# Optimization experiments

Hardware: AMD Instinct MI355X
Metric: run time of the kernel (lower is better)

## Reference

```python
import jax, jax.numpy as jnp
import numpy as np

D_MODEL = 1024
N_HEADS = 16


def setup_inputs() -> dict:
    key = jax.random.key(0)
    ks = jax.random.split(key, 5)
    B, T, C = 4, 2048, D_MODEL
    x = jax.random.normal(ks[0], (B, T, C), dtype=jnp.float32)
    W_attn = jax.random.normal(ks[1], (C, 3 * C), dtype=jnp.float32) * (1.0 / np.sqrt(C))
    b_attn = jnp.zeros((3 * C,), dtype=jnp.float32)
    W_proj = jax.random.normal(ks[2], (C, C), dtype=jnp.float32) * (1.0 / np.sqrt(C))
    b_proj = jnp.zeros((C,), dtype=jnp.float32)
    return {"x": x, "W_attn": W_attn, "b_attn": b_attn, "W_proj": W_proj, "b_proj": b_proj}


def reference(x, W_attn, b_attn, W_proj, b_proj):
    B, T, C = x.shape
    H = N_HEADS
    hd = C // H
    qkv = x @ W_attn + b_attn                      # [B,T,3C]
    q, k, v = jnp.split(qkv, 3, axis=2)
    # [B,T,C] -> [B,H,T,hd]
    q = q.reshape(B, T, H, hd).transpose(0, 2, 1, 3)
    k = k.reshape(B, T, H, hd).transpose(0, 2, 1, 3)
    v = v.reshape(B, T, H, hd).transpose(0, 2, 1, 3)
    scale = 1.0 / jnp.sqrt(jnp.float32(hd))
    attn = jnp.einsum('bhqd,bhkd->bhqk', q, k) * scale
    causal = jnp.tril(jnp.ones((T, T), dtype=bool))
    attn = jnp.where(causal[None, None], attn, -jnp.inf)
    w = jax.nn.softmax(attn, axis=-1)
    ctx = jnp.einsum('bhqk,bhkd->bhqd', w, v)      # [B,H,T,hd]
    ctx = ctx.transpose(0, 2, 1, 3).reshape(B, T, C)
    return ctx @ W_proj + b_proj
```

## Files before the change

### kernel.cpp

```cpp
#include <hip/hip_runtime.h>
#include <hip/hip_bf16.h>

typedef __bf16 bf16x8 __attribute__((ext_vector_type(8)));
typedef __bf16 bf16x4 __attribute__((ext_vector_type(4)));
typedef float f32x4 __attribute__((ext_vector_type(4)));

#define MFMA(A, B, C) __builtin_amdgcn_mfma_f32_16x16x32_bf16((A), (B), (C), 0, 0, 0)

#if __has_builtin(__builtin_amdgcn_exp2f)
#define EXP2(x) __builtin_amdgcn_exp2f(x)
#else
#define EXP2(x) exp2f(x)
#endif

#define T_SEQ 2048
#define BATCH 4
#define CDIM  1024
#define HEADS 16
#define HD    64
#define MROWS (BATCH * T_SEQ)
#define QK_SCALE 0.18033688011112042f
#define KTILES (CDIM / 64)

__device__ __forceinline__ void async_ld16(const __bf16* g, __bf16* l) {
    __builtin_amdgcn_global_load_lds(
        (const __attribute__((address_space(1))) void*)g,
        (__attribute__((address_space(3))) void*)l, 16, 0, 0);
}

__global__ __launch_bounds__(256) void conv_transpose(const float* __restrict__ src,
                                                      __bf16* __restrict__ dst,
                                                      int R, int C)
{
    __shared__ float tile[32][33];
    int c0 = blockIdx.x * 32, r0 = blockIdx.y * 32;
    int tx = threadIdx.x, ty = threadIdx.y;
#pragma unroll
    for (int i = 0; i < 4; i++)
        tile[ty + i * 8][tx] = src[(long)(r0 + ty + i * 8) * C + c0 + tx];
    __syncthreads();
#pragma unroll
    for (int i = 0; i < 4; i++)
        dst[(long)(c0 + ty + i * 8) * R + r0 + tx] = (__bf16)tile[tx][ty + i * 8];
}

__global__ __launch_bounds__(256) void conv_bf16(const float* __restrict__ src,
                                                 __bf16* __restrict__ dst)
{
    long i = ((long)blockIdx.x * 256 + threadIdx.x) * 8;
    f32x4 f0 = ((const f32x4*)(src + i))[0];
    f32x4 f1 = ((const f32x4*)(src + i))[1];
    bf16x8 v;
#pragma unroll
    for (int j = 0; j < 4; j++) { v[j] = (__bf16)f0[j]; v[4 + j] = (__bf16)f1[j]; }
    *(bf16x8*)(dst + i) = v;
}

__global__ __launch_bounds__(256) void vtrans(const __bf16* __restrict__ qkv,
                                              __bf16* __restrict__ vt)
{
    __shared__ __bf16 tile[32][33];
    int bh = blockIdx.z;
    int b = bh >> 4, h = bh & 15;
    int t0 = blockIdx.x * 32, d0 = blockIdx.y * 32;
    int tx = threadIdx.x, ty = threadIdx.y;
#pragma unroll
    for (int i = 0; i < 4; i++)
        tile[ty + i * 8][tx] =
            qkv[(long)(b * T_SEQ + t0 + ty + i * 8) * (3 * CDIM) + 2 * CDIM + h * HD + d0 + tx];
    __syncthreads();
#pragma unroll
    for (int i = 0; i < 4; i++)
        vt[(long)(bh * HD + d0 + ty + i * 8) * T_SEQ + t0 + tx] = tile[tx][ty + i * 8];
}


#define QS_ALO(p, kt)                                                            \
    do {                                                                         \
        async_ld16(Asrc + (long)(kt) * 64, &Ab[p][sdst]);                        \
        async_ld16(Asrc + (long)128 * CDIM + (kt) * 64, &Ab[p][8192 + sdst]);    \
    } while (0)
#define QS_AHI(p, kt)                                                            \
    do {                                                                         \
        async_ld16(Asrc + (long)64 * CDIM + (kt) * 64, &Ab[p][4096 + sdst]);     \
        async_ld16(Asrc + (long)192 * CDIM + (kt) * 64, &Ab[p][12288 + sdst]);   \
    } while (0)
#define QS_B(p, kt)                                                              \
    do {                                                                         \
        async_ld16(Bsrc + (long)(kt) * 64, &Bb[p][sdst]);                        \
        async_ld16(Bsrc + (long)64 * CDIM + (kt) * 64, &Bb[p][4096 + sdst]);     \
        async_ld16(Bsrc + (long)128 * CDIM + (kt) * 64, &Bb[p][8192 + sdst]);    \
    } while (0)

__global__ __launch_bounds__(512, 2) void gemm_qkv(const __bf16* __restrict__ A,
                                                   const __bf16* __restrict__ Bt,
                                                   const float* __restrict__ bias,
                                                   __bf16* __restrict__ C)
{
    __shared__ __attribute__((aligned(16))) __bf16 Ab[2][256 * 64];
    __shared__ __attribute__((aligned(16))) __bf16 Bb[2][192 * 64];

    const int bid = (int)blockIdx.x;
    const int swz = (bid & 7) * 64 + (bid >> 3);
    const int n0 = (swz & 15) * 192;
    const int m0 = (swz >> 4) * 256;

    const int t = threadIdx.x;
    const int wave = t >> 6, lane = t & 63;
    const int quad = lane >> 4, l15 = lane & 15;
    const int wm = wave >> 2, wn = wave & 3;

    const int srow = t >> 3;
    const int scol = ((t & 7) * 8) ^ ((srow & 7) << 3);
    const int sdst = srow * 64 + (t & 7) * 8;
    const __bf16* Asrc = A + (long)(m0 + srow) * CDIM + scol;
    const __bf16* Bsrc = Bt + (long)(n0 + srow) * CDIM + scol;

    const int kx0 = (quad * 8) ^ ((l15 & 7) << 3);
    const int kx1 = (32 + quad * 8) ^ ((l15 & 7) << 3);
    const int aro = (wm * 128 + l15) * 64;
    const int bro = (wn * 48 + l15) * 64;

    f32x4 acc[8][3] = {};
    bf16x8 A0[4][2], A1[4][2], B0[2][2], B1[2];

    QS_ALO(0, 0); QS_AHI(0, 0); QS_B(0, 0);
    QS_ALO(1, 1); QS_AHI(1, 1); QS_B(1, 1);
    asm volatile("s_waitcnt vmcnt(7)" ::: "memory");
    __builtin_amdgcn_s_barrier();
#pragma unroll
    for (int mf = 0; mf < 4; mf++) {
        A0[mf][0] = *(const bf16x8*)&Ab[0][aro + mf * 1024 + kx0];
        A0[mf][1] = *(const bf16x8*)&Ab[0][aro + mf * 1024 + kx1];
    }
#pragma unroll
    for (int nf = 0; nf < 2; nf++) {
        B0[nf][0] = *(const bf16x8*)&Bb[0][bro + nf * 1024 + kx0];
        B0[nf][1] = *(const bf16x8*)&Bb[0][bro + nf * 1024 + kx1];
    }

#pragma unroll 2
    for (int kt = 0; kt < KTILES; ++kt) {
        const int cur = kt & 1, nxt = cur ^ 1;

#pragma unroll
        for (int mf = 0; mf < 4; mf++) {
            A1[mf][0] = *(const bf16x8*)&Ab[cur][aro + 4096 + mf * 1024 + kx0];
            A1[mf][1] = *(const bf16x8*)&Ab[cur][aro + 4096 + mf * 1024 + kx1];
        }
        __builtin_amdgcn_s_barrier();
        asm volatile("s_waitcnt lgkmcnt(8)");
        __builtin_amdgcn_sched_barrier(0);
        __builtin_amdgcn_s_setprio(1);
#pragma unroll
        for (int mf = 0; mf < 4; mf++)
#pragma unroll
            for (int nf = 0; nf < 2; nf++) {
                acc[mf][nf] = MFMA(A0[mf][0], B0[nf][0], acc[mf][nf]);
                acc[mf][nf] = MFMA(A0[mf][1], B0[nf][1], acc[mf][nf]);
            }
        __builtin_amdgcn_s_setprio(0);
        __builtin_amdgcn_s_barrier();

        B1[0] = *(const bf16x8*)&Bb[cur][bro + 2048 + kx0];
        B1[1] = *(const bf16x8*)&Bb[cur][bro + 2048 + kx1];
        if (kt + 2 < KTILES) QS_ALO(cur, kt + 2);
        __builtin_amdgcn_s_barrier();
        asm volatile("s_waitcnt lgkmcnt(2)");
        __builtin_amdgcn_sched_barrier(0);
        __builtin_amdgcn_s_setprio(1);
#pragma unroll
        for (int mf = 0; mf < 4; mf++)
#pragma unroll
            for (int nf = 0; nf < 2; nf++) {
                acc[4 + mf][nf] = MFMA(A1[mf][0], B0[nf][0], acc[4 + mf][nf]);
                acc[4 + mf][nf] = MFMA(A1[mf][1], B0[nf][1], acc[4 + mf][nf]);
            }
        __builtin_amdgcn_s_setprio(0);
        if (kt + 2 < KTILES) { asm volatile("s_waitcnt vmcnt(2)" ::: "memory"); }
        else                 { asm volatile("s_waitcnt vmcnt(0)" ::: "memory"); }
        __builtin_amdgcn_s_barrier();

        if (kt + 2 < KTILES) QS_AHI(cur, kt + 2);
        if (kt + 1 < KTILES) {
#pragma unroll
            for (int nf = 0; nf < 2; nf++) {
                B0[nf][0] = *(const bf16x8*)&Bb[nxt][bro + nf * 1024 + kx0];
                B0[nf][1] = *(const bf16x8*)&Bb[nxt][bro + nf * 1024 + kx1];
            }
        }
        __builtin_amdgcn_s_barrier();
        asm volatile("s_waitcnt lgkmcnt(4)");
        __builtin_amdgcn_sched_barrier(0);
        __builtin_amdgcn_s_setprio(1);
#pragma unroll
        for (int mf = 0; mf < 4; mf++) {
            acc[mf][2] = MFMA(A0[mf][0], B1[0], acc[mf][2]);
            acc[mf][2] = MFMA(A0[mf][1], B1[1], acc[mf][2]);
        }
        __builtin_amdgcn_s_setprio(0);
        __builtin_amdgcn_s_barrier();

        if (kt + 2 < KTILES) QS_B(cur, kt + 2);
        if (kt + 1 < KTILES) {
#pragma unroll
            for (int mf = 0; mf < 4; mf++) {
                A0[mf][0] = *(const bf16x8*)&Ab[nxt][aro + mf * 1024 + kx0];
                A0[mf][1] = *(const bf16x8*)&Ab[nxt][aro + mf * 1024 + kx1];
            }
        }
        __builtin_amdgcn_s_barrier();
        asm volatile("s_waitcnt lgkmcnt(8)");
        __builtin_amdgcn_sched_barrier(0);
        __builtin_amdgcn_s_setprio(1);
#pragma unroll
        for (int mf = 0; mf < 4; mf++) {
            acc[4 + mf][2] = MFMA(A1[mf][0], B1[0], acc[4 + mf][2]);
            acc[4 + mf][2] = MFMA(A1[mf][1], B1[1], acc[4 + mf][2]);
        }
        __builtin_amdgcn_s_setprio(0);
        __builtin_amdgcn_s_barrier();
    }

#pragma unroll
    for (int mf = 0; mf < 8; mf++) {
#pragma unroll
        for (int nf = 0; nf < 3; nf++) {
            const int col = n0 + wn * 48 + nf * 16 + l15;
            const float bv = bias[col];
            const float sc = (col < CDIM) ? QK_SCALE : 1.0f;
#pragma unroll
            for (int r = 0; r < 4; r++) {
                const int row = m0 + wm * 128 + (mf >> 2) * 64 + (mf & 3) * 16 + quad * 4 + r;
                C[(long)row * (3 * CDIM) + col] = (__bf16)((acc[mf][nf][r] + bv) * sc);
            }
        }
    }
}

#define PS_A(p, kt)                                                              \
    do {                                                                         \
        async_ld16(Asrc + (long)(kt) * 64, &Ab[p][sdst]);                        \
        async_ld16(Asrc + (long)64 * (3 * CDIM) + (kt) * 64, &Ab[p][4096 + sdst]); \
    } while (0)
#define PS_B(p, kt)                                                              \
    do {                                                                         \
        async_ld16(Bsrc + (long)(kt) * 64, &Bb[p][sdst]);                        \
        async_ld16(Bsrc + (long)64 * CDIM + (kt) * 64, &Bb[p][4096 + sdst]);     \
        async_ld16(Bsrc + (long)128 * CDIM + (kt) * 64, &Bb[p][8192 + sdst]);    \
        async_ld16(Bsrc + (long)192 * CDIM + (kt) * 64, &Bb[p][12288 + sdst]);   \
    } while (0)

__global__ __launch_bounds__(512, 2) void gemm_proj(const __bf16* __restrict__ A,
                                                    const __bf16* __restrict__ Bt,
                                                    const float* __restrict__ bias,
                                                    float* __restrict__ C)
{
    __shared__ __attribute__((aligned(16))) __bf16 Ab[2][128 * 64];
    __shared__ __attribute__((aligned(16))) __bf16 Bb[2][256 * 64];

    const int bid = (int)blockIdx.x;
    const int swz = (bid & 7) * 32 + (bid >> 3);
    const int n0 = (swz & 3) * 256;
    const int m0 = (swz >> 2) * 128;

    const int t = threadIdx.x;
    const int wave = t >> 6, lane = t & 63;
    const int quad = lane >> 4, l15 = lane & 15;
    const int wm = wave >> 2, wn = wave & 3;

    const int srow = t >> 3;
    const int scol = ((t & 7) * 8) ^ ((srow & 7) << 3);
    const int sdst = srow * 64 + (t & 7) * 8;
    const __bf16* Asrc = A + (long)(m0 + srow) * (3 * CDIM) + scol;
    const __bf16* Bsrc = Bt + (long)(n0 + srow) * CDIM + scol;

    const int kx0 = (quad * 8) ^ ((l15 & 7) << 3);
    const int kx1 = (32 + quad * 8) ^ ((l15 & 7) << 3);
    const int aro = (wm * 64 + l15) * 64;
    const int bro = (wn * 64 + l15) * 64;

    f32x4 acc[4][4] = {};
    bf16x8 A0[2][2], A1[2][2], B0[2][2], B1[2][2];

    PS_A(0, 0); PS_B(0, 0);
    PS_A(1, 1); PS_B(1, 1);
    asm volatile("s_waitcnt vmcnt(6)" ::: "memory");
    __builtin_amdgcn_s_barrier();
#pragma unroll
    for (int mf = 0; mf < 2; mf++) {
        A0[mf][0] = *(const bf16x8*)&Ab[0][aro + mf * 1024 + kx0];
        A0[mf][1] = *(const bf16x8*)&Ab[0][aro + mf * 1024 + kx1];
    }
#pragma unroll
    for (int nf = 0; nf < 2; nf++) {
        B0[nf][0] = *(const bf16x8*)&Bb[0][bro + nf * 1024 + kx0];
        B0[nf][1] = *(const bf16x8*)&Bb[0][bro + nf * 1024 + kx1];
    }

#pragma unroll 2
    for (int kt = 0; kt < KTILES; ++kt) {
        const int cur = kt & 1, nxt = cur ^ 1;

#pragma unroll
        for (int mf = 0; mf < 2; mf++) {
            A1[mf][0] = *(const bf16x8*)&Ab[cur][aro + 2048 + mf * 1024 + kx0];
            A1[mf][1] = *(const bf16x8*)&Ab[cur][aro + 2048 + mf * 1024 + kx1];
        }
        __builtin_amdgcn_s_barrier();
        asm volatile("s_waitcnt lgkmcnt(4)");
        __builtin_amdgcn_sched_barrier(0);
        __builtin_amdgcn_s_setprio(1);
#pragma unroll
        for (int mf = 0; mf < 2; mf++)
#pragma unroll
            for (int nf = 0; nf < 2; nf++) {
                acc[mf][nf] = MFMA(A0[mf][0], B0[nf][0], acc[mf][nf]);
                acc[mf][nf] = MFMA(A0[mf][1], B0[nf][1], acc[mf][nf]);
            }
        __builtin_amdgcn_s_setprio(0);
        __builtin_amdgcn_s_barrier();

#pragma unroll
        for (int nf = 0; nf < 2; nf++) {
            B1[nf][0] = *(const bf16x8*)&Bb[cur][bro + 2048 + nf * 1024 + kx0];
            B1[nf][1] = *(const bf16x8*)&Bb[cur][bro + 2048 + nf * 1024 + kx1];
        }
        __builtin_amdgcn_s_barrier();
        asm volatile("s_waitcnt lgkmcnt(4)");
        __builtin_amdgcn_sched_barrier(0);
        __builtin_amdgcn_s_setprio(1);
#pragma unroll
        for (int mf = 0; mf < 2; mf++)
#pragma unroll
            for (int nf = 0; nf < 2; nf++) {
                acc[2 + mf][nf] = MFMA(A1[mf][0], B0[nf][0], acc[2 + mf][nf]);
                acc[2 + mf][nf] = MFMA(A1[mf][1], B0[nf][1], acc[2 + mf][nf]);
            }
        __builtin_amdgcn_s_setprio(0);
        asm volatile("s_waitcnt vmcnt(0)" ::: "memory");
        __builtin_amdgcn_s_barrier();

        if (kt + 2 < KTILES) PS_A(cur, kt + 2);
        if (kt + 1 < KTILES) {
#pragma unroll
            for (int nf = 0; nf < 2; nf++) {
                B0[nf][0] = *(const bf16x8*)&Bb[nxt][bro + nf * 1024 + kx0];
                B0[nf][1] = *(const bf16x8*)&Bb[nxt][bro + nf * 1024 + kx1];
            }
        }
        __builtin_amdgcn_s_barrier();
        asm volatile("s_waitcnt lgkmcnt(4)");
        __builtin_amdgcn_sched_barrier(0);
        __builtin_amdgcn_s_setprio(1);
#pragma unroll
        for (int mf = 0; mf < 2; mf++)
#pragma unroll
            for (int nf = 0; nf < 2; nf++) {
                acc[mf][2 + nf] = MFMA(A0[mf][0], B1[nf][0], acc[mf][2 + nf]);
                acc[mf][2 + nf] = MFMA(A0[mf][1], B1[nf][1], acc[mf][2 + nf]);
            }
        __builtin_amdgcn_s_setprio(0);
        __builtin_amdgcn_s_barrier();

        if (kt + 2 < KTILES) PS_B(cur, kt + 2);
        if (kt + 1 < KTILES) {
#pragma unroll
            for (int mf = 0; mf < 2; mf++) {
                A0[mf][0] = *(const bf16x8*)&Ab[nxt][aro + mf * 1024 + kx0];
                A0[mf][1] = *(const bf16x8*)&Ab[nxt][aro + mf * 1024 + kx1];
            }
        }
        __builtin_amdgcn_s_barrier();
        asm volatile("s_waitcnt lgkmcnt(4)");
        __builtin_amdgcn_sched_barrier(0);
        __builtin_amdgcn_s_setprio(1);
#pragma unroll
        for (int mf = 0; mf < 2; mf++)
#pragma unroll
            for (int nf = 0; nf < 2; nf++) {
                acc[2 + mf][2 + nf] = MFMA(A1[mf][0], B1[nf][0], acc[2 + mf][2 + nf]);
                acc[2 + mf][2 + nf] = MFMA(A1[mf][1], B1[nf][1], acc[2 + mf][2 + nf]);
            }
        __builtin_amdgcn_s_setprio(0);
        __builtin_amdgcn_s_barrier();
    }

#pragma unroll
    for (int mf = 0; mf < 4; mf++) {
#pragma unroll
        for (int nf = 0; nf < 4; nf++) {
            const int col = n0 + wn * 64 + (nf >> 1) * 32 + (nf & 1) * 16 + l15;
            const float bv = bias[col];
#pragma unroll
            for (int r = 0; r < 4; r++) {
                const int row = m0 + wm * 64 + (mf >> 1) * 32 + (mf & 1) * 16 + quad * 4 + r;
                C[(long)row * CDIM + col] = acc[mf][nf][r] + bv;
            }
        }
    }
}

__global__ __launch_bounds__(256) void attn_kernel(__bf16* qkv,
                                                   const __bf16* __restrict__ vt)
{
    __shared__ __attribute__((aligned(16))) __bf16 Ks[2][64 * 32];
    __shared__ __attribute__((aligned(16))) __bf16 Vts[2][64 * 32];
    __shared__ __attribute__((aligned(16))) __bf16 Ps[8][16 * 72];

    const int bh = blockIdx.x;
    const int b = bh >> 4, h = bh & 15;
    const int qt = (int)gridDim.y - 1 - (int)blockIdx.y;
    const int q0 = qt * 128;
    const int t = threadIdx.x;
    const int wave = t >> 6, lane = t & 63;
    const int quad = lane >> 4, l15 = lane & 15;

    bf16x8 qfr[2][2];
#pragma unroll
    for (int f = 0; f < 2; f++) {
        const __bf16* qb = qkv + (long)(b * T_SEQ + q0 + f * 64 + wave * 16 + l15) * (3 * CDIM) + h * HD;
        qfr[f][0] = *(const bf16x8*)(qb + quad * 8);
        qfr[f][1] = *(const bf16x8*)(qb + 32 + quad * 8);
    }

    bf16x8 vone;
#pragma unroll
    for (int j = 0; j < 8; j++) vone[j] = (__bf16)1.0f;

    f32x4 Oacc[2][4] = {};
    f32x4 lacc[2] = {};

    const __bf16* kbase = qkv + (long)(b * T_SEQ + (t >> 2)) * (3 * CDIM)
                          + CDIM + h * HD + (t & 3) * 8;
    const __bf16* vbase = vt + ((long)bh * HD + (t >> 2)) * T_SEQ + (t & 3) * 8;

    const int ntiles = (q0 + 128) / 64;
    for (int kt = 0; kt < ntiles; kt++) {
        const __bf16* kp = kbase + (long)kt * 64 * (3 * CDIM);
        async_ld16(kp,      &Ks[0][t * 8]);
        async_ld16(kp + 32, &Ks[1][t * 8]);
        const __bf16* vp = vbase + kt * 64;
        async_ld16(vp,      &Vts[0][t * 8]);
        async_ld16(vp + 32, &Vts[1][t * 8]);
        __syncthreads();

#pragma unroll
        for (int c = 0; c < 4; c++) {
            bf16x8 kf0 = *(const bf16x8*)&Ks[0][(c * 16 + l15) * 32 + quad * 8];
            bf16x8 kf1 = *(const bf16x8*)&Ks[1][(c * 16 + l15) * 32 + quad * 8];
#pragma unroll
            for (int f = 0; f < 2; f++) {
                f32x4 z = {};
                z = MFMA(kf0, qfr[f][0], z);
                z = MFMA(kf1, qfr[f][1], z);
                const int qbf = q0 + f * 64 + wave * 16;
                const int qg = qbf + l15;
                const int kvb = kt * 64 + c * 16 + quad * 4;
                bf16x4 pk;
                if (kt * 64 + 63 > qbf) {
#pragma unroll
                    for (int r = 0; r < 4; r++) {
                        float v = (kvb + r > qg) ? -1e30f : z[r];
                        pk[r] = (__bf16)EXP2(v);
                    }
                } else {
#pragma unroll
                    for (int r = 0; r < 4; r++)
                        pk[r] = (__bf16)EXP2(z[r]);
                }
                *(bf16x4*)&Ps[wave * 2 + f][l15 * 72 + c * 16 + quad * 4] = pk;
            }
        }

        __threadfence_block();

        bf16x8 pf[2][2];
#pragma unroll
        for (int f = 0; f < 2; f++) {
            pf[f][0] = *(const bf16x8*)&Ps[wave * 2 + f][l15 * 72 + quad * 8];
            pf[f][1] = *(const bf16x8*)&Ps[wave * 2 + f][l15 * 72 + 32 + quad * 8];
            lacc[f] = MFMA(pf[f][0], vone, lacc[f]);
            lacc[f] = MFMA(pf[f][1], vone, lacc[f]);
        }
#pragma unroll
        for (int n = 0; n < 4; n++) {
            bf16x8 vf0 = *(const bf16x8*)&Vts[0][(n * 16 + l15) * 32 + quad * 8];
            bf16x8 vf1 = *(const bf16x8*)&Vts[1][(n * 16 + l15) * 32 + quad * 8];
#pragma unroll
            for (int f = 0; f < 2; f++) {
                Oacc[f][n] = MFMA(pf[f][0], vf0, Oacc[f][n]);
                Oacc[f][n] = MFMA(pf[f][1], vf1, Oacc[f][n]);
            }
        }
        __syncthreads();
    }

#pragma unroll
    for (int f = 0; f < 2; f++)
#pragma unroll
        for (int n = 0; n < 4; n++) {
            int col = h * HD + n * 16 + l15;
#pragma unroll
            for (int r = 0; r < 4; r++) {
                int row = q0 + f * 64 + wave * 16 + quad * 4 + r;
                float val = Oacc[f][n][r] / lacc[f][r];
                qkv[(long)(b * T_SEQ + row) * (3 * CDIM) + col] = (__bf16)val;
            }
        }
}

extern "C" void kernel_launch(void* const* d_in, const int* in_sizes, int n_in,
                              void* d_out, int out_size, void* d_ws, size_t ws_size,
                              hipStream_t stream) {
    (void)in_sizes; (void)n_in; (void)out_size; (void)ws_size;
    const float* x  = (const float*)d_in[0];
    const float* Wa = (const float*)d_in[1];
    const float* ba = (const float*)d_in[2];
    const float* Wp = (const float*)d_in[3];
    const float* bp = (const float*)d_in[4];
    float* out = (float*)d_out;

    char* ws = (char*)d_ws;
    __bf16* qkv = (__bf16*)(ws);
    __bf16* Wat = (__bf16*)(ws + 50331648);
    __bf16* vt  = (__bf16*)(ws + 50331648);
    __bf16* Wpt = (__bf16*)(ws + 50331648);
    __bf16* xbf = (__bf16*)d_out;

    conv_bf16<<<dim3(MROWS * CDIM / (256 * 8)), 256, 0, stream>>>(x, xbf);
    conv_transpose<<<dim3(3 * CDIM / 32, CDIM / 32), dim3(32, 8), 0, stream>>>(Wa, Wat, CDIM, 3 * CDIM);

    gemm_qkv<<<dim3(512), 512, 0, stream>>>(xbf, Wat, ba, qkv);

    vtrans<<<dim3(T_SEQ / 32, HD / 32, BATCH * HEADS), dim3(32, 8), 0, stream>>>(qkv, vt);

    attn_kernel<<<dim3(BATCH * HEADS, T_SEQ / 128), 256, 0, stream>>>(qkv, vt);

    conv_transpose<<<dim3(CDIM / 32, CDIM / 32), dim3(32, 8), 0, stream>>>(Wp, Wpt, CDIM, CDIM);

    gemm_proj<<<dim3(256), 512, 0, stream>>>(qkv, Wpt, bp, out);
}
```

Baseline: 258.2 us.

## Double-buffer K/V tiles in attention with swizzled LDS and causal tile skipping

The attention kernel now prefetches the next K/V tile into a second LDS buffer while computing on the current one, using explicit vmcnt waits and raw barriers in place of __syncthreads. The LDS layout changes to 64-wide rows with an XOR swizzle to avoid bank conflicts, and the P scratch drops its padding. Per-wave causal checks skip QK^T MFMAs and PV work for fully masked 16-row subblocks and write zeros for masked P chunks. This aims to hide global load latency and cut wasted compute on the causal diagonal, at the cost of doubled K/V LDS use and reliance on hand-counted vmcnt values.

```diff
diff --git a/kernel.cpp b/kernel.cpp
--- a/kernel.cpp
+++ b/kernel.cpp
@@ -401,12 +401,22 @@
     }
 }
 
+#define ATT_STAGE(p, kt_)                                                        \
+    do {                                                                         \
+        const __bf16* kp_ = kglob + (long)(kt_) * 64 * (3 * CDIM);               \
+        async_ld16(kp_, &Ks[p][t * 8]);                                          \
+        async_ld16(kp_ + (long)32 * (3 * CDIM), &Ks[p][t * 8 + 2048]);           \
+        const __bf16* vp_ = vglob + (kt_) * 64;                                  \
+        async_ld16(vp_, &Vts[p][t * 8]);                                         \
+        async_ld16(vp_ + (long)32 * T_SEQ, &Vts[p][t * 8 + 2048]);               \
+    } while (0)
+
 __global__ __launch_bounds__(256) void attn_kernel(__bf16* qkv,
                                                    const __bf16* __restrict__ vt)
 {
-    __shared__ __attribute__((aligned(16))) __bf16 Ks[2][64 * 32];
-    __shared__ __attribute__((aligned(16))) __bf16 Vts[2][64 * 32];
-    __shared__ __attribute__((aligned(16))) __bf16 Ps[8][16 * 72];
+    __shared__ __attribute__((aligned(16))) __bf16 Ks[2][64 * 64];
+    __shared__ __attribute__((aligned(16))) __bf16 Vts[2][64 * 64];
+    __shared__ __attribute__((aligned(16))) __bf16 Ps[8][16 * 64];
 
     const int bh = blockIdx.x;
     const int b = bh >> 4, h = bh & 15;
@@ -416,6 +426,14 @@
     const int wave = t >> 6, lane = t & 63;
     const int quad = lane >> 4, l15 = lane & 15;
 
+    const int srow = t >> 3;
+    const int scol = (((t & 7) ^ (srow & 7)) << 3);
+    const __bf16* kglob = qkv + (long)(b * T_SEQ + srow) * (3 * CDIM) + CDIM + h * HD + scol;
+    const __bf16* vglob = vt + ((long)bh * HD + srow) * T_SEQ + scol;
+
+    const int kx0 = (quad * 8) ^ ((l15 & 7) << 3);
+    const int kx1 = (32 + quad * 8) ^ ((l15 & 7) << 3);
+
     bf16x8 qfr[2][2];
 #pragma unroll
     for (int f = 0; f < 2; f++) {
@@ -431,34 +449,45 @@
     f32x4 Oacc[2][4] = {};
     f32x4 lacc[2] = {};
 
-    const __bf16* kbase = qkv + (long)(b * T_SEQ + (t >> 2)) * (3 * CDIM)
-                          + CDIM + h * HD + (t & 3) * 8;
-    const __bf16* vbase = vt + ((long)bh * HD + (t >> 2)) * T_SEQ + (t & 3) * 8;
-
+    const int qb0 = q0 + wave * 16;
     const int ntiles = (q0 + 128) / 64;
+
+    ATT_STAGE(0, 0);
     for (int kt = 0; kt < ntiles; kt++) {
-        const __bf16* kp = kbase + (long)kt * 64 * (3 * CDIM);
-        async_ld16(kp,      &Ks[0][t * 8]);
-        async_ld16(kp + 32, &Ks[1][t * 8]);
-        const __bf16* vp = vbase + kt * 64;
-        async_ld16(vp,      &Vts[0][t * 8]);
-        async_ld16(vp + 32, &Vts[1][t * 8]);
-        __syncthreads();
+        const int cur = kt & 1;
+        const int kv0 = kt * 64;
+        if (kt + 1 < ntiles) {
+            ATT_STAGE(cur ^ 1, kt + 1);
+            asm volatile("s_waitcnt vmcnt(4)" ::: "memory");
+        } else {
+            asm volatile("s_waitcnt vmcnt(0)" ::: "memory");
+        }
+        __builtin_amdgcn_s_barrier();
+        asm volatile("" ::: "memory");
 
 #pragma unroll
         for (int c = 0; c < 4; c++) {
-            bf16x8 kf0 = *(const bf16x8*)&Ks[0][(c * 16 + l15) * 32 + quad * 8];
-            bf16x8 kf1 = *(const bf16x8*)&Ks[1][(c * 16 + l15) * 32 + quad * 8];
+            const int rk = c * 16 + l15;
+            bf16x8 kf0 = *(const bf16x8*)&Ks[cur][rk * 64 + kx0];
+            bf16x8 kf1 = *(const bf16x8*)&Ks[cur][rk * 64 + kx1];
 #pragma unroll
             for (int f = 0; f < 2; f++) {
+                const int qbf = qb0 + f * 64;
+                if (kv0 > qbf + 15) continue;
+                __bf16* pdst = &Ps[wave * 2 + f][l15 * 64 +
+                                ((((c * 2 + (quad >> 1)) ^ (l15 & 7)) << 3) + (quad & 1) * 4)];
+                if (kv0 + c * 16 > qbf + 15) {
+                    bf16x4 zz = {};
+                    *(bf16x4*)pdst = zz;
+                    continue;
+                }
                 f32x4 z = {};
                 z = MFMA(kf0, qfr[f][0], z);
                 z = MFMA(kf1, qfr[f][1], z);
-                const int qbf = q0 + f * 64 + wave * 16;
-                const int qg = qbf + l15;
-                const int kvb = kt * 64 + c * 16 + quad * 4;
                 bf16x4 pk;
-                if (kt * 64 + 63 > qbf) {
+                if (kv0 + 63 > qbf) {
+                    const int qg = qbf + l15;
+                    const int kvb = kv0 + c * 16 + quad * 4;
 #pragma unroll
                     for (int r = 0; r < 4; r++) {
                         float v = (kvb + r > qg) ? -1e30f : z[r];
@@ -469,31 +498,36 @@
                     for (int r = 0; r < 4; r++)
                         pk[r] = (__bf16)EXP2(z[r]);
                 }
-                *(bf16x4*)&Ps[wave * 2 + f][l15 * 72 + c * 16 + quad * 4] = pk;
+                *(bf16x4*)pdst = pk;
             }
         }
 
         __threadfence_block();
 
+        const bool act0 = (kv0 <= qb0 + 15);
         bf16x8 pf[2][2];
 #pragma unroll
         for (int f = 0; f < 2; f++) {
-            pf[f][0] = *(const bf16x8*)&Ps[wave * 2 + f][l15 * 72 + quad * 8];
-            pf[f][1] = *(const bf16x8*)&Ps[wave * 2 + f][l15 * 72 + 32 + quad * 8];
+            if (f == 0 && !act0) continue;
+            pf[f][0] = *(const bf16x8*)&Ps[wave * 2 + f][l15 * 64 + kx0];
+            pf[f][1] = *(const bf16x8*)&Ps[wave * 2 + f][l15 * 64 + kx1];
             lacc[f] = MFMA(pf[f][0], vone, lacc[f]);
             lacc[f] = MFMA(pf[f][1], vone, lacc[f]);
         }
 #pragma unroll
         for (int n = 0; n < 4; n++) {
-            bf16x8 vf0 = *(const bf16x8*)&Vts[0][(n * 16 + l15) * 32 + quad * 8];
-            bf16x8 vf1 = *(const bf16x8*)&Vts[1][(n * 16 + l15) * 32 + quad * 8];
-#pragma unroll
-            for (int f = 0; f < 2; f++) {
-                Oacc[f][n] = MFMA(pf[f][0], vf0, Oacc[f][n]);
-                Oacc[f][n] = MFMA(pf[f][1], vf1, Oacc[f][n]);
-            }
-        }
-        __syncthreads();
+            const int rv = n * 16 + l15;
+            bf16x8 vf0 = *(const bf16x8*)&Vts[cur][rv * 64 + kx0];
+            bf16x8 vf1 = *(const bf16x8*)&Vts[cur][rv * 64 + kx1];
+            if (act0) {
+                Oacc[0][n] = MFMA(pf[0][0], vf0, Oacc[0][n]);
+                Oacc[0][n] = MFMA(pf[0][1], vf1, Oacc[0][n]);
+            }
+            Oacc[1][n] = MFMA(pf[1][0], vf0, Oacc[1][n]);
+            Oacc[1][n] = MFMA(pf[1][1], vf1, Oacc[1][n]);
+        }
+        __builtin_amdgcn_s_barrier();
+        asm volatile("" ::: "memory");
     }
 
 #pragma unroll
```

After: 262.3 us. About the same (+1.6%).

## Fuse input conversions into one launch and write V transposed from QKV GEMM

Applied to the files above, without the earlier changes.

Merges the x fp32-to-bf16 conversion and the W_attn transpose-convert into a single prep kernel, placing the transposed weights in the output buffer so they no longer share workspace with vt. The QKV GEMM epilogue now writes V tiles directly in transposed [b,h,d,t] layout as 4-element vector stores, which removes the separate vtrans kernel and its extra read and write of V. This saves one launch and a full pass over V, at the cost of a divergent epilogue and strided stores for V columns.

```diff
diff --git a/kernel.cpp b/kernel.cpp
--- a/kernel.cpp
+++ b/kernel.cpp
@@ -28,6 +28,35 @@
         (__attribute__((address_space(3))) void*)l, 16, 0, 0);
 }
 
+__global__ __launch_bounds__(256) void prep(const float* __restrict__ x,
+                                            __bf16* __restrict__ xbf,
+                                            const float* __restrict__ Wa,
+                                            __bf16* __restrict__ Wat)
+{
+    __shared__ float tile[32][33];
+    const int bid = blockIdx.x;
+    if (bid < 4096) {
+        long i = ((long)bid * 256 + threadIdx.x) * 8;
+        f32x4 f0 = ((const f32x4*)(x + i))[0];
+        f32x4 f1 = ((const f32x4*)(x + i))[1];
+        bf16x8 v;
+#pragma unroll
+        for (int j = 0; j < 4; j++) { v[j] = (__bf16)f0[j]; v[4 + j] = (__bf16)f1[j]; }
+        *(bf16x8*)(xbf + i) = v;
+    } else {
+        const int bb = bid - 4096;
+        const int tx = threadIdx.x & 31, ty = threadIdx.x >> 5;
+        const int c0 = (bb % 96) * 32, r0 = (bb / 96) * 32;
+#pragma unroll
+        for (int i = 0; i < 4; i++)
+            tile[ty + i * 8][tx] = Wa[(long)(r0 + ty + i * 8) * (3 * CDIM) + c0 + tx];
+        __syncthreads();
+#pragma unroll
+        for (int i = 0; i < 4; i++)
+            Wat[(long)(c0 + ty + i * 8) * CDIM + r0 + tx] = (__bf16)tile[tx][ty + i * 8];
+    }
+}
+
 __global__ __launch_bounds__(256) void conv_transpose(const float* __restrict__ src,
                                                       __bf16* __restrict__ dst,
                                                       int R, int C)
@@ -42,36 +71,6 @@
 #pragma unroll
     for (int i = 0; i < 4; i++)
         dst[(long)(c0 + ty + i * 8) * R + r0 + tx] = (__bf16)tile[tx][ty + i * 8];
-}
-
-__global__ __launch_bounds__(256) void conv_bf16(const float* __restrict__ src,
-                                                 __bf16* __restrict__ dst)
-{
-    long i = ((long)blockIdx.x * 256 + threadIdx.x) * 8;
-    f32x4 f0 = ((const f32x4*)(src + i))[0];
-    f32x4 f1 = ((const f32x4*)(src + i))[1];
-    bf16x8 v;
-#pragma unroll
-    for (int j = 0; j < 4; j++) { v[j] = (__bf16)f0[j]; v[4 + j] = (__bf16)f1[j]; }
-    *(bf16x8*)(dst + i) = v;
-}
-
-__global__ __launch_bounds__(256) void vtrans(const __bf16* __restrict__ qkv,
-                                              __bf16* __restrict__ vt)
-{
-    __shared__ __bf16 tile[32][33];
-    int bh = blockIdx.z;
-    int b = bh >> 4, h = bh & 15;
-    int t0 = blockIdx.x * 32, d0 = blockIdx.y * 32;
-    int tx = threadIdx.x, ty = threadIdx.y;
-#pragma unroll
-    for (int i = 0; i < 4; i++)
-        tile[ty + i * 8][tx] =
-            qkv[(long)(b * T_SEQ + t0 + ty + i * 8) * (3 * CDIM) + 2 * CDIM + h * HD + d0 + tx];
-    __syncthreads();
-#pragma unroll
-    for (int i = 0; i < 4; i++)
-        vt[(long)(bh * HD + d0 + ty + i * 8) * T_SEQ + t0 + tx] = tile[tx][ty + i * 8];
 }
 
 
@@ -95,7 +94,8 @@
 __global__ __launch_bounds__(512, 2) void gemm_qkv(const __bf16* __restrict__ A,
                                                    const __bf16* __restrict__ Bt,
                                                    const float* __restrict__ bias,
-                                                   __bf16* __restrict__ C)
+                                                   __bf16* __restrict__ C,
+                                                   __bf16* __restrict__ vt)
 {
     __shared__ __attribute__((aligned(16))) __bf16 Ab[2][256 * 64];
     __shared__ __attribute__((aligned(16))) __bf16 Bb[2][192 * 64];
@@ -222,17 +222,29 @@
         __builtin_amdgcn_s_barrier();
     }
 
+    const int bB = m0 >> 11;
+    const int tb = (m0 & (T_SEQ - 1)) + wm * 128;
 #pragma unroll
     for (int mf = 0; mf < 8; mf++) {
 #pragma unroll
         for (int nf = 0; nf < 3; nf++) {
-            const int col = n0 + wn * 48 + nf * 16 + l15;
+            const int colb = n0 + wn * 48 + nf * 16;
+            const int col = colb + l15;
             const float bv = bias[col];
-            const float sc = (col < CDIM) ? QK_SCALE : 1.0f;
-#pragma unroll
-            for (int r = 0; r < 4; r++) {
-                const int row = m0 + wm * 128 + (mf >> 2) * 64 + (mf & 3) * 16 + quad * 4 + r;
-                C[(long)row * (3 * CDIM) + col] = (__bf16)((acc[mf][nf][r] + bv) * sc);
+            if (colb >= 2 * CDIM) {
+                __bf16* vdst = vt + (long)(bB * CDIM + col - 2 * CDIM) * T_SEQ
+                             + tb + (mf >> 2) * 64 + (mf & 3) * 16 + quad * 4;
+                bf16x4 pv;
+#pragma unroll
+                for (int r = 0; r < 4; r++) pv[r] = (__bf16)(acc[mf][nf][r] + bv);
+                *(bf16x4*)vdst = pv;
+            } else {
+                const float sc = (col < CDIM) ? QK_SCALE : 1.0f;
+#pragma unroll
+                for (int r = 0; r < 4; r++) {
+                    const int row = m0 + wm * 128 + (mf >> 2) * 64 + (mf & 3) * 16 + quad * 4 + r;
+                    C[(long)row * (3 * CDIM) + col] = (__bf16)((acc[mf][nf][r] + bv) * sc);
+                }
             }
         }
     }
@@ -523,17 +535,14 @@
 
     char* ws = (char*)d_ws;
     __bf16* qkv = (__bf16*)(ws);
-    __bf16* Wat = (__bf16*)(ws + 50331648);
     __bf16* vt  = (__bf16*)(ws + 50331648);
     __bf16* Wpt = (__bf16*)(ws + 50331648);
     __bf16* xbf = (__bf16*)d_out;
-
-    conv_bf16<<<dim3(MROWS * CDIM / (256 * 8)), 256, 0, stream>>>(x, xbf);
-    conv_transpose<<<dim3(3 * CDIM / 32, CDIM / 32), dim3(32, 8), 0, stream>>>(Wa, Wat, CDIM, 3 * CDIM);
-
-    gemm_qkv<<<dim3(512), 512, 0, stream>>>(xbf, Wat, ba, qkv);
-
-    vtrans<<<dim3(T_SEQ / 32, HD / 32, BATCH * HEADS), dim3(32, 8), 0, stream>>>(qkv, vt);
+    __bf16* Wat = (__bf16*)((char*)d_out + 16777216);
+
+    prep<<<dim3(4096 + 3072), 256, 0, stream>>>(x, xbf, Wa, Wat);
+
+    gemm_qkv<<<dim3(512), 512, 0, stream>>>(xbf, Wat, ba, qkv, vt);
 
     attn_kernel<<<dim3(BATCH * HEADS, T_SEQ / 128), 256, 0, stream>>>(qkv, vt);
 
```

Result: faster. 249.8 us (-3.3%).
